# Kernel optimization log

Measured on AMD Instinct MI355X. Metric: run time of the kernel, lower is better.

## Reference

```python
import jax, jax.numpy as jnp
import numpy as np


def setup_inputs() -> dict:
    key = jax.random.key(0)
    kq, kk, kv = jax.random.split(key, 3)
    B, H, S, D = 2, 16, 2048, 64
    return {
        "queries": jax.random.normal(kq, (B, H, S, D), dtype=jnp.float32),
        "keys": jax.random.normal(kk, (B, H, S, D), dtype=jnp.float32),
        "values": jax.random.normal(kv, (B, H, S, D), dtype=jnp.float32),
        "d_k": D,
    }


def reference(queries, keys, values, d_k):
    # scores = Q K^T / sqrt(d_k)  -> [B, H, S, S]
    scale = 1.0 / jnp.sqrt(jnp.asarray(d_k, dtype=queries.dtype))
    scores = jnp.einsum("bhqd,bhkd->bhqk", queries, keys) * scale
    weights = jax.nn.softmax(scores, axis=-1)
    return jnp.einsum("bhqk,bhkd->bhqd", weights, values)
```

## Files before the change

kernel.cpp:

```cpp
#include <hip/hip_runtime.h>


typedef _Float16 half8 __attribute__((ext_vector_type(8)));
typedef _Float16 half4 __attribute__((ext_vector_type(4)));
typedef float floatx4 __attribute__((ext_vector_type(4)));

constexpr int BQ = 128;
constexpr int BK = 64;
constexpr int DH = 64;
constexpr int SLEN = 2048;
constexpr int NT = SLEN / BK;
constexpr int THREADS = 256;

#define MFMA16(a, b, c) __builtin_amdgcn_mfma_f32_16x16x32_f16(a, b, c, 0, 0, 0)

__global__ __launch_bounds__(256)
void prep_kv(const float* __restrict__ K, const float* __restrict__ V,
             _Float16* __restrict__ Kh, _Float16* __restrict__ Vt)
{
    __shared__ _Float16 t[64 * 72];
    const int tid  = threadIdx.x;
    const int tile = blockIdx.x & 31;
    const int head = blockIdx.x >> 5;
    const size_t base = ((size_t)head * SLEN + tile * 64) * DH;

    {
        const float4* src = (const float4*)(K + base);
        half8* dst = (half8*)(Kh + base);
        #pragma unroll
        for (int r = 0; r < 2; r++) {
            int i = tid + 256 * r;
            float4 a = src[2 * i], b = src[2 * i + 1];
            half8 h;
            h[0] = (_Float16)a.x; h[1] = (_Float16)a.y;
            h[2] = (_Float16)a.z; h[3] = (_Float16)a.w;
            h[4] = (_Float16)b.x; h[5] = (_Float16)b.y;
            h[6] = (_Float16)b.z; h[7] = (_Float16)b.w;
            dst[i] = h;
        }
    }
    {
        const float4* src = (const float4*)(V + base);
        #pragma unroll
        for (int r = 0; r < 4; r++) {
            int i = tid + 256 * r, row = i >> 4, g = i & 15;
            float4 a = src[row * 16 + g];
            half4 h;
            h[0] = (_Float16)a.x; h[1] = (_Float16)a.y;
            h[2] = (_Float16)a.z; h[3] = (_Float16)a.w;
            *(half4*)&t[row * 72 + g * 4] = h;
        }
        __syncthreads();
        _Float16* dst = Vt + (size_t)head * DH * SLEN + tile * 64;
        #pragma unroll
        for (int r = 0; r < 2; r++) {
            int i = tid + 256 * r, d = i >> 3, g = i & 7;
            half8 h;
            #pragma unroll
            for (int j = 0; j < 8; j++) h[j] = t[(g * 8 + j) * 72 + d];
            *(half8*)&dst[(size_t)d * SLEN + g * 8] = h;
        }
    }
}

__global__ __launch_bounds__(THREADS, 2)
void attn_f16_mfma(const float* __restrict__ Q, const _Float16* __restrict__ Kh,
                   const _Float16* __restrict__ Vt, float* __restrict__ Out,
                   const int* __restrict__ dkp)
{
    __shared__ __align__(16) float xbuf[2][64][76];

    const int tid  = threadIdx.x;
    const int wave = tid >> 6;
    const int lane = tid & 63;
    const int quad = lane >> 4;
    const int n16  = lane & 15;
    const int wm   = wave & 1;
    const int wn   = wave >> 1;

    const int id   = blockIdx.x;
    const int xcd  = id & 7;
    const int slot = id >> 3;
    const int head = xcd * 4 + (slot >> 4);
    const int qt   = slot & 15;

    const float scale2 = rsqrtf((float)(*dkp)) * 1.44269504088896340736f;
    const size_t headoff = (size_t)head * SLEN * DH;

    half8 qB[4][2];
    {
        const float4* Qg = (const float4*)(Q + headoff + (size_t)qt * BQ * DH);
        #pragma unroll
        for (int rg = 0; rg < 4; rg++)
            #pragma unroll
            for (int kd = 0; kd < 2; kd++) {
                int row = wn * 64 + rg * 16 + n16;
                float4 a = Qg[row * 16 + kd * 8 + quad * 2];
                float4 b = Qg[row * 16 + kd * 8 + quad * 2 + 1];
                half8 h;
                h[0] = (_Float16)(a.x * scale2); h[1] = (_Float16)(a.y * scale2);
                h[2] = (_Float16)(a.z * scale2); h[3] = (_Float16)(a.w * scale2);
                h[4] = (_Float16)(b.x * scale2); h[5] = (_Float16)(b.y * scale2);
                h[6] = (_Float16)(b.z * scale2); h[7] = (_Float16)(b.w * scale2);
                qB[rg][kd] = h;
            }
    }

    const _Float16* Khh = Kh + headoff;
    const _Float16* Vth = Vt + (size_t)head * DH * SLEN;

    const int krow = wm * 32 + (n16 >> 2) * 8 + (n16 & 3);

#define LOADK(KT, DST) do {                                                    \
    const _Float16* p_ = Khh + (size_t)(KT) * BK * DH;                         \
    _Pragma("unroll") for (int kd_ = 0; kd_ < 2; kd_++)                        \
    _Pragma("unroll") for (int c_ = 0; c_ < 2; c_++)                           \
        DST[kd_][c_] = *(const half8*)                                         \
            &p_[(size_t)(krow + c_ * 4) * DH + kd_ * 32 + quad * 8];           \
} while (0)

#define LOADV(KT) do {                                                         \
    _Pragma("unroll") for (int c2_ = 0; c2_ < 4; c2_++)                        \
        vA[c2_] = *(const half8*)                                              \
            &Vth[(size_t)(c2_ * 16 + n16) * SLEN + (KT) * BK + wm * 32 + quad * 8]; \
} while (0)

    floatx4 oacc[4][4];
    float lsumv[4];
    const floatx4 fz = {0.f, 0.f, 0.f, 0.f};
    #pragma unroll
    for (int rg = 0; rg < 4; rg++) {
        lsumv[rg] = 0.f;
        #pragma unroll
        for (int c2 = 0; c2 < 4; c2++) oacc[rg][c2] = fz;
    }

    half8 kAa[2][2], kAb[2][2], vA[4], pB[4];
    LOADK(0, kAa);

#define TILE(KT, KA, KN) do {                                                  \
    LOADV(KT);                                                                 \
    LOADK((KT) + 1, KN);                                                       \
    __builtin_amdgcn_sched_barrier(0);                                         \
    _Pragma("unroll") for (int rg = 0; rg < 4; rg++) {                         \
        floatx4 s0 = MFMA16(KA[0][0], qB[rg][0], fz);                          \
        s0 = MFMA16(KA[1][0], qB[rg][1], s0);                                  \
        floatx4 s1 = MFMA16(KA[0][1], qB[rg][0], fz);                          \
        s1 = MFMA16(KA[1][1], qB[rg][1], s1);                                  \
        float e0 = exp2f(s0[0]), e1 = exp2f(s0[1]);                            \
        float e2 = exp2f(s0[2]), e3 = exp2f(s0[3]);                            \
        float e4 = exp2f(s1[0]), e5 = exp2f(s1[1]);                            \
        float e6 = exp2f(s1[2]), e7 = exp2f(s1[3]);                            \
        pB[rg][0] = (_Float16)e0; pB[rg][1] = (_Float16)e1;                    \
        pB[rg][2] = (_Float16)e2; pB[rg][3] = (_Float16)e3;                    \
        pB[rg][4] = (_Float16)e4; pB[rg][5] = (_Float16)e5;                    \
        pB[rg][6] = (_Float16)e6; pB[rg][7] = (_Float16)e7;                    \
        lsumv[rg] += ((e0 + e1) + (e2 + e3)) + ((e4 + e5) + (e6 + e7));        \
    }                                                                          \
    __builtin_amdgcn_s_setprio(1);                                             \
    _Pragma("unroll") for (int rg = 0; rg < 4; rg++)                           \
    _Pragma("unroll") for (int c2 = 0; c2 < 4; c2++)                           \
        oacc[rg][c2] = MFMA16(vA[c2], pB[rg], oacc[rg][c2]);                   \
    __builtin_amdgcn_s_setprio(0);                                             \
} while (0)

    for (int kt = 0; kt < NT; kt += 2) {
        TILE(kt,     kAa, kAb);
        TILE(kt + 1, kAb, kAa);
    }

    if (wm) {
        float* b = &xbuf[wn][lane][0];
        #pragma unroll
        for (int rg = 0; rg < 4; rg++)
            #pragma unroll
            for (int c2 = 0; c2 < 4; c2++)
                *(floatx4*)&b[rg * 16 + c2 * 4] = oacc[rg][c2];
        #pragma unroll
        for (int rg = 0; rg < 4; rg++) b[64 + rg] = lsumv[rg];
    }
    __syncthreads();
    if (!wm) {
        const float* b = &xbuf[wn][lane][0];
        #pragma unroll
        for (int rg = 0; rg < 4; rg++) {
            #pragma unroll
            for (int c2 = 0; c2 < 4; c2++)
                oacc[rg][c2] += *(const floatx4*)&b[rg * 16 + c2 * 4];
            lsumv[rg] += b[64 + rg];
            lsumv[rg] += __shfl_xor(lsumv[rg], 16, 64);
            lsumv[rg] += __shfl_xor(lsumv[rg], 32, 64);
        }
        float* Og = Out + headoff + (size_t)qt * BQ * DH;
        #pragma unroll
        for (int rg = 0; rg < 4; rg++) {
            float inv = 1.0f / lsumv[rg];
            int row = wn * 64 + rg * 16 + n16;
            #pragma unroll
            for (int c2 = 0; c2 < 4; c2++) {
                floatx4 v = oacc[rg][c2];
                float4 w = make_float4(v[0] * inv, v[1] * inv, v[2] * inv, v[3] * inv);
                *(float4*)&Og[row * 64 + c2 * 16 + quad * 4] = w;
            }
        }
    }
}

extern "C" void kernel_launch(void* const* d_in, const int* in_sizes, int n_in,
                              void* d_out, int out_size, void* d_ws, size_t ws_size,
                              hipStream_t stream) {
    const float* Q = (const float*)d_in[0];
    const float* K = (const float*)d_in[1];
    const float* V = (const float*)d_in[2];
    const int*  dk = (const int*)d_in[3];
    float* Out = (float*)d_out;

    const int nbh  = in_sizes[0] / (SLEN * DH);
    const size_t n = (size_t)nbh * SLEN * DH;

    _Float16* Kh = (_Float16*)d_ws;
    _Float16* Vt = Kh + n;

    prep_kv<<<nbh * 32, 256, 0, stream>>>(K, V, Kh, Vt);

    dim3 grid(nbh * (SLEN / BQ));
    attn_f16_mfma<<<grid, THREADS, 0, stream>>>(Q, Kh, Vt, Out, dk);
}
```

Before: 159.8 us.

## Split query tile across eight waves and drop K double-buffering

Doubles the block to 512 threads so each wave handles 32 query rows instead of 64, halving per-wave accumulators and Q registers and raising the occupancy target. The K double-buffer is removed: K and V for each tile are now loaded at the top of the iteration, just before use. This is meant to improve latency hiding through more waves, at the cost of exposing load latency inside each wave and doubling K/V loads per block. The kernel launch block size must change to match; that part is not visible here.

```diff
diff --git a/kernel.cpp b/kernel.cpp
--- a/kernel.cpp
+++ b/kernel.cpp
@@ -10,7 +10,7 @@
 constexpr int DH = 64;
 constexpr int SLEN = 2048;
 constexpr int NT = SLEN / BK;
-constexpr int THREADS = 256;
+constexpr int THREADS = 512;
 
 #define MFMA16(a, b, c) __builtin_amdgcn_mfma_f32_16x16x32_f16(a, b, c, 0, 0, 0)
 
@@ -63,12 +63,12 @@
     }
 }
 
-__global__ __launch_bounds__(THREADS, 2)
+__global__ __launch_bounds__(THREADS, 4)
 void attn_f16_mfma(const float* __restrict__ Q, const _Float16* __restrict__ Kh,
                    const _Float16* __restrict__ Vt, float* __restrict__ Out,
                    const int* __restrict__ dkp)
 {
-    __shared__ __align__(16) float xbuf[2][64][76];
+    __shared__ __align__(16) float xbuf[4][64][36];
 
     const int tid  = threadIdx.x;
     const int wave = tid >> 6;
@@ -87,14 +87,14 @@
     const float scale2 = rsqrtf((float)(*dkp)) * 1.44269504088896340736f;
     const size_t headoff = (size_t)head * SLEN * DH;
 
-    half8 qB[4][2];
+    half8 qB[2][2];
     {
         const float4* Qg = (const float4*)(Q + headoff + (size_t)qt * BQ * DH);
         #pragma unroll
-        for (int rg = 0; rg < 4; rg++)
+        for (int rg = 0; rg < 2; rg++)
             #pragma unroll
             for (int kd = 0; kd < 2; kd++) {
-                int row = wn * 64 + rg * 16 + n16;
+                int row = wn * 32 + rg * 16 + n16;
                 float4 a = Qg[row * 16 + kd * 8 + quad * 2];
                 float4 b = Qg[row * 16 + kd * 8 + quad * 2 + 1];
                 half8 h;
@@ -111,11 +111,11 @@
 
     const int krow = wm * 32 + (n16 >> 2) * 8 + (n16 & 3);
 
-#define LOADK(KT, DST) do {                                                    \
+#define LOADK(KT) do {                                                         \
     const _Float16* p_ = Khh + (size_t)(KT) * BK * DH;                         \
     _Pragma("unroll") for (int kd_ = 0; kd_ < 2; kd_++)                        \
     _Pragma("unroll") for (int c_ = 0; c_ < 2; c_++)                           \
-        DST[kd_][c_] = *(const half8*)                                         \
+        kA[kd_][c_] = *(const half8*)                                          \
             &p_[(size_t)(krow + c_ * 4) * DH + kd_ * 32 + quad * 8];           \
 } while (0)
 
@@ -125,77 +125,81 @@
             &Vth[(size_t)(c2_ * 16 + n16) * SLEN + (KT) * BK + wm * 32 + quad * 8]; \
 } while (0)
 
-    floatx4 oacc[4][4];
-    float lsumv[4];
+    floatx4 oacc[2][4];
+    float lsumv[2];
     const floatx4 fz = {0.f, 0.f, 0.f, 0.f};
     #pragma unroll
-    for (int rg = 0; rg < 4; rg++) {
+    for (int rg = 0; rg < 2; rg++) {
         lsumv[rg] = 0.f;
         #pragma unroll
         for (int c2 = 0; c2 < 4; c2++) oacc[rg][c2] = fz;
     }
 
-    half8 kAa[2][2], kAb[2][2], vA[4], pB[4];
-    LOADK(0, kAa);
-
-#define TILE(KT, KA, KN) do {                                                  \
-    LOADV(KT);                                                                 \
-    LOADK((KT) + 1, KN);                                                       \
-    __builtin_amdgcn_sched_barrier(0);                                         \
-    _Pragma("unroll") for (int rg = 0; rg < 4; rg++) {                         \
-        floatx4 s0 = MFMA16(KA[0][0], qB[rg][0], fz);                          \
-        s0 = MFMA16(KA[1][0], qB[rg][1], s0);                                  \
-        floatx4 s1 = MFMA16(KA[0][1], qB[rg][0], fz);                          \
-        s1 = MFMA16(KA[1][1], qB[rg][1], s1);                                  \
-        float e0 = exp2f(s0[0]), e1 = exp2f(s0[1]);                            \
-        float e2 = exp2f(s0[2]), e3 = exp2f(s0[3]);                            \
-        float e4 = exp2f(s1[0]), e5 = exp2f(s1[1]);                            \
-        float e6 = exp2f(s1[2]), e7 = exp2f(s1[3]);                            \
-        pB[rg][0] = (_Float16)e0; pB[rg][1] = (_Float16)e1;                    \
-        pB[rg][2] = (_Float16)e2; pB[rg][3] = (_Float16)e3;                    \
-        pB[rg][4] = (_Float16)e4; pB[rg][5] = (_Float16)e5;                    \
-        pB[rg][6] = (_Float16)e6; pB[rg][7] = (_Float16)e7;                    \
-        lsumv[rg] += ((e0 + e1) + (e2 + e3)) + ((e4 + e5) + (e6 + e7));        \
-    }                                                                          \
-    __builtin_amdgcn_s_setprio(1);                                             \
-    _Pragma("unroll") for (int rg = 0; rg < 4; rg++)                           \
-    _Pragma("unroll") for (int c2 = 0; c2 < 4; c2++)                           \
-        oacc[rg][c2] = MFMA16(vA[c2], pB[rg], oacc[rg][c2]);                   \
-    __builtin_amdgcn_s_setprio(0);                                             \
-} while (0)
-
-    for (int kt = 0; kt < NT; kt += 2) {
-        TILE(kt,     kAa, kAb);
-        TILE(kt + 1, kAb, kAa);
+    half8 kA[2][2], vA[4], pB[2];
+
+    for (int kt = 0; kt < NT; ++kt) {
+        LOADK(kt);
+        LOADV(kt);
+        __builtin_amdgcn_sched_barrier(0);
+
+        floatx4 sC[2][2];
+        #pragma unroll
+        for (int rg = 0; rg < 2; rg++)
+            #pragma unroll
+            for (int c = 0; c < 2; c++) {
+                floatx4 acc = MFMA16(kA[0][c], qB[rg][0], fz);
+                sC[rg][c] = MFMA16(kA[1][c], qB[rg][1], acc);
+            }
+
+        #pragma unroll
+        for (int rg = 0; rg < 2; rg++) {
+            float e0 = exp2f(sC[rg][0][0]), e1 = exp2f(sC[rg][0][1]);
+            float e2 = exp2f(sC[rg][0][2]), e3 = exp2f(sC[rg][0][3]);
+            float e4 = exp2f(sC[rg][1][0]), e5 = exp2f(sC[rg][1][1]);
+            float e6 = exp2f(sC[rg][1][2]), e7 = exp2f(sC[rg][1][3]);
+            pB[rg][0] = (_Float16)e0; pB[rg][1] = (_Float16)e1;
+            pB[rg][2] = (_Float16)e2; pB[rg][3] = (_Float16)e3;
+            pB[rg][4] = (_Float16)e4; pB[rg][5] = (_Float16)e5;
+            pB[rg][6] = (_Float16)e6; pB[rg][7] = (_Float16)e7;
+            lsumv[rg] += ((e0 + e1) + (e2 + e3)) + ((e4 + e5) + (e6 + e7));
+        }
+
+        __builtin_amdgcn_s_setprio(1);
+        #pragma unroll
+        for (int rg = 0; rg < 2; rg++)
+            #pragma unroll
+            for (int c2 = 0; c2 < 4; c2++)
+                oacc[rg][c2] = MFMA16(vA[c2], pB[rg], oacc[rg][c2]);
+        __builtin_amdgcn_s_setprio(0);
     }
 
     if (wm) {
         float* b = &xbuf[wn][lane][0];
         #pragma unroll
-        for (int rg = 0; rg < 4; rg++)
+        for (int rg = 0; rg < 2; rg++)
             #pragma unroll
             for (int c2 = 0; c2 < 4; c2++)
                 *(floatx4*)&b[rg * 16 + c2 * 4] = oacc[rg][c2];
         #pragma unroll
-        for (int rg = 0; rg < 4; rg++) b[64 + rg] = lsumv[rg];
+        for (int rg = 0; rg < 2; rg++) b[32 + rg] = lsumv[rg];
     }
     __syncthreads();
     if (!wm) {
         const float* b = &xbuf[wn][lane][0];
         #pragma unroll
-        for (int rg = 0; rg < 4; rg++) {
+        for (int rg = 0; rg < 2; rg++) {
             #pragma unroll
             for (int c2 = 0; c2 < 4; c2++)
                 oacc[rg][c2] += *(const floatx4*)&b[rg * 16 + c2 * 4];
-            lsumv[rg] += b[64 + rg];
+            lsumv[rg] += b[32 + rg];
             lsumv[rg] += __shfl_xor(lsumv[rg], 16, 64);
             lsumv[rg] += __shfl_xor(lsumv[rg], 32, 64);
         }
         float* Og = Out + headoff + (size_t)qt * BQ * DH;
         #pragma unroll
-        for (int rg = 0; rg < 4; rg++) {
+        for (int rg = 0; rg < 2; rg++) {
             float inv = 1.0f / lsumv[rg];
-            int row = wn * 64 + rg * 16 + n16;
+            int row = wn * 32 + rg * 16 + n16;
             #pragma unroll
             for (int c2 = 0; c2 < 4; c2++) {
                 floatx4 v = oacc[rg][c2];
```

After: 211.7 us. 32.5% more time.

## Halve query tile, raise occupancy, MFMA row sums, double-buffer V, packed fp16 convert

Applied to the files above, without the earlier changes.

Shrinks the query tile from 128 to 64 rows per block, doubling the grid and requesting three blocks per SIMD instead of two so more waves can hide latency. Row sums of the softmax numerator now come from an extra MFMA against a vector of ones instead of scalar adds and shuffles. V tiles are double-buffered and prefetched one tile ahead alongside K, and exp results are packed to fp16 with cvt_pkrtz. In exchange, each K/V tile is reused across fewer query rows, which raises global/L2 traffic, and the prefetch wraps to tile 0 on the last iteration, a redundant load.

```diff
diff --git a/kernel.cpp b/kernel.cpp
--- a/kernel.cpp
+++ b/kernel.cpp
@@ -3,9 +3,10 @@
 
 typedef _Float16 half8 __attribute__((ext_vector_type(8)));
 typedef _Float16 half4 __attribute__((ext_vector_type(4)));
+typedef __fp16 fp16x2 __attribute__((ext_vector_type(2)));
 typedef float floatx4 __attribute__((ext_vector_type(4)));
 
-constexpr int BQ = 128;
+constexpr int BQ = 64;
 constexpr int BK = 64;
 constexpr int DH = 64;
 constexpr int SLEN = 2048;
@@ -63,12 +64,12 @@
     }
 }
 
-__global__ __launch_bounds__(THREADS, 2)
+__global__ __launch_bounds__(THREADS, 3)
 void attn_f16_mfma(const float* __restrict__ Q, const _Float16* __restrict__ Kh,
                    const _Float16* __restrict__ Vt, float* __restrict__ Out,
                    const int* __restrict__ dkp)
 {
-    __shared__ __align__(16) float xbuf[2][64][76];
+    __shared__ __align__(16) float xbuf[2][64][36];
 
     const int tid  = threadIdx.x;
     const int wave = tid >> 6;
@@ -81,20 +82,20 @@
     const int id   = blockIdx.x;
     const int xcd  = id & 7;
     const int slot = id >> 3;
-    const int head = xcd * 4 + (slot >> 4);
-    const int qt   = slot & 15;
+    const int head = xcd * 4 + (slot >> 5);
+    const int qt   = slot & 31;
 
     const float scale2 = rsqrtf((float)(*dkp)) * 1.44269504088896340736f;
     const size_t headoff = (size_t)head * SLEN * DH;
 
-    half8 qB[4][2];
+    half8 qB[2][2];
     {
         const float4* Qg = (const float4*)(Q + headoff + (size_t)qt * BQ * DH);
         #pragma unroll
-        for (int rg = 0; rg < 4; rg++)
+        for (int rg = 0; rg < 2; rg++)
             #pragma unroll
             for (int kd = 0; kd < 2; kd++) {
-                int row = wn * 64 + rg * 16 + n16;
+                int row = wn * 32 + rg * 16 + n16;
                 float4 a = Qg[row * 16 + kd * 8 + quad * 2];
                 float4 b = Qg[row * 16 + kd * 8 + quad * 2 + 1];
                 half8 h;
@@ -119,83 +120,90 @@
             &p_[(size_t)(krow + c_ * 4) * DH + kd_ * 32 + quad * 8];           \
 } while (0)
 
-#define LOADV(KT) do {                                                         \
+#define LOADV(KT, DST) do {                                                    \
     _Pragma("unroll") for (int c2_ = 0; c2_ < 4; c2_++)                        \
-        vA[c2_] = *(const half8*)                                              \
+        DST[c2_] = *(const half8*)                                             \
             &Vth[(size_t)(c2_ * 16 + n16) * SLEN + (KT) * BK + wm * 32 + quad * 8]; \
 } while (0)
 
-    floatx4 oacc[4][4];
-    float lsumv[4];
+    floatx4 oacc[2][4];
+    floatx4 lsum[2];
     const floatx4 fz = {0.f, 0.f, 0.f, 0.f};
     #pragma unroll
-    for (int rg = 0; rg < 4; rg++) {
-        lsumv[rg] = 0.f;
+    for (int rg = 0; rg < 2; rg++) {
+        lsum[rg] = fz;
         #pragma unroll
         for (int c2 = 0; c2 < 4; c2++) oacc[rg][c2] = fz;
     }
-
-    half8 kAa[2][2], kAb[2][2], vA[4], pB[4];
-    LOADK(0, kAa);
-
-#define TILE(KT, KA, KN) do {                                                  \
-    LOADV(KT);                                                                 \
-    LOADK((KT) + 1, KN);                                                       \
+    half8 ones;
+    #pragma unroll
+    for (int j = 0; j < 8; j++) ones[j] = (_Float16)1.0f;
+
+    half8 kAa[2][2], kAb[2][2], vAa[4], vAb[4], pB[2];
+
+    union PU { fp16x2 h2[4]; half8 h8; };
+
+#define TILE(KT, KA, VA, KN, VN) do {                                          \
+    int ktn_ = ((KT) + 1 < NT) ? (KT) + 1 : 0;                                 \
+    LOADK(ktn_, KN);                                                           \
+    LOADV(ktn_, VN);                                                           \
     __builtin_amdgcn_sched_barrier(0);                                         \
-    _Pragma("unroll") for (int rg = 0; rg < 4; rg++) {                         \
-        floatx4 s0 = MFMA16(KA[0][0], qB[rg][0], fz);                          \
-        s0 = MFMA16(KA[1][0], qB[rg][1], s0);                                  \
-        floatx4 s1 = MFMA16(KA[0][1], qB[rg][0], fz);                          \
-        s1 = MFMA16(KA[1][1], qB[rg][1], s1);                                  \
-        float e0 = exp2f(s0[0]), e1 = exp2f(s0[1]);                            \
-        float e2 = exp2f(s0[2]), e3 = exp2f(s0[3]);                            \
-        float e4 = exp2f(s1[0]), e5 = exp2f(s1[1]);                            \
-        float e6 = exp2f(s1[2]), e7 = exp2f(s1[3]);                            \
-        pB[rg][0] = (_Float16)e0; pB[rg][1] = (_Float16)e1;                    \
-        pB[rg][2] = (_Float16)e2; pB[rg][3] = (_Float16)e3;                    \
-        pB[rg][4] = (_Float16)e4; pB[rg][5] = (_Float16)e5;                    \
-        pB[rg][6] = (_Float16)e6; pB[rg][7] = (_Float16)e7;                    \
-        lsumv[rg] += ((e0 + e1) + (e2 + e3)) + ((e4 + e5) + (e6 + e7));        \
+    floatx4 sC[2][2];                                                          \
+    _Pragma("unroll") for (int rg = 0; rg < 2; rg++)                           \
+    _Pragma("unroll") for (int c = 0; c < 2; c++) {                            \
+        floatx4 acc = MFMA16(KA[0][c], qB[rg][0], fz);                         \
+        sC[rg][c] = MFMA16(KA[1][c], qB[rg][1], acc);                          \
+    }                                                                          \
+    _Pragma("unroll") for (int rg = 0; rg < 2; rg++) {                         \
+        PU u_;                                                                 \
+        u_.h2[0] = __builtin_amdgcn_cvt_pkrtz(exp2f(sC[rg][0][0]),             \
+                                              exp2f(sC[rg][0][1]));            \
+        u_.h2[1] = __builtin_amdgcn_cvt_pkrtz(exp2f(sC[rg][0][2]),             \
+                                              exp2f(sC[rg][0][3]));            \
+        u_.h2[2] = __builtin_amdgcn_cvt_pkrtz(exp2f(sC[rg][1][0]),             \
+                                              exp2f(sC[rg][1][1]));            \
+        u_.h2[3] = __builtin_amdgcn_cvt_pkrtz(exp2f(sC[rg][1][2]),             \
+                                              exp2f(sC[rg][1][3]));            \
+        pB[rg] = u_.h8;                                                        \
     }                                                                          \
     __builtin_amdgcn_s_setprio(1);                                             \
-    _Pragma("unroll") for (int rg = 0; rg < 4; rg++)                           \
-    _Pragma("unroll") for (int c2 = 0; c2 < 4; c2++)                           \
-        oacc[rg][c2] = MFMA16(vA[c2], pB[rg], oacc[rg][c2]);                   \
+    _Pragma("unroll") for (int rg = 0; rg < 2; rg++) {                         \
+        lsum[rg] = MFMA16(ones, pB[rg], lsum[rg]);                             \
+        _Pragma("unroll") for (int c2 = 0; c2 < 4; c2++)                       \
+            oacc[rg][c2] = MFMA16(VA[c2], pB[rg], oacc[rg][c2]);               \
+    }                                                                          \
     __builtin_amdgcn_s_setprio(0);                                             \
 } while (0)
 
+    LOADK(0, kAa);
+    LOADV(0, vAa);
+
     for (int kt = 0; kt < NT; kt += 2) {
-        TILE(kt,     kAa, kAb);
-        TILE(kt + 1, kAb, kAa);
+        TILE(kt,     kAa, vAa, kAb, vAb);
+        TILE(kt + 1, kAb, vAb, kAa, vAa);
     }
 
     if (wm) {
         float* b = &xbuf[wn][lane][0];
         #pragma unroll
-        for (int rg = 0; rg < 4; rg++)
+        for (int rg = 0; rg < 2; rg++)
             #pragma unroll
             for (int c2 = 0; c2 < 4; c2++)
                 *(floatx4*)&b[rg * 16 + c2 * 4] = oacc[rg][c2];
         #pragma unroll
-        for (int rg = 0; rg < 4; rg++) b[64 + rg] = lsumv[rg];
+        for (int rg = 0; rg < 2; rg++) b[32 + rg] = lsum[rg][0];
     }
     __syncthreads();
     if (!wm) {
         const float* b = &xbuf[wn][lane][0];
-        #pragma unroll
-        for (int rg = 0; rg < 4; rg++) {
+        float* Og = Out + headoff + (size_t)qt * BQ * DH;
+        #pragma unroll
+        for (int rg = 0; rg < 2; rg++) {
             #pragma unroll
             for (int c2 = 0; c2 < 4; c2++)
                 oacc[rg][c2] += *(const floatx4*)&b[rg * 16 + c2 * 4];
-            lsumv[rg] += b[64 + rg];
-            lsumv[rg] += __shfl_xor(lsumv[rg], 16, 64);
-            lsumv[rg] += __shfl_xor(lsumv[rg], 32, 64);
-        }
-        float* Og = Out + headoff + (size_t)qt * BQ * DH;
-        #pragma unroll
-        for (int rg = 0; rg < 4; rg++) {
-            float inv = 1.0f / lsumv[rg];
-            int row = wn * 64 + rg * 16 + n16;
+            float inv = 1.0f / (lsum[rg][0] + b[32 + rg]);
+            int row = wn * 32 + rg * 16 + n16;
             #pragma unroll
             for (int c2 = 0; c2 < 4; c2++) {
                 floatx4 v = oacc[rg][c2];
```

Measured after the change: 213.7 us. 1.34x slower.
